# Kernel tuning notes

Hardware: AMD Instinct MI355X
Metric: run time of the kernel (lower is better)

The kernel has to match this reference:

```python
import jax, jax.numpy as jnp
import numpy as np

N, T, C, H = 32, 512, 768, 1536  # batch, seq_len, dim, int(dim*expand)


def setup_inputs() -> dict:
    key = jax.random.key(0)
    ks = jax.random.split(key, 10)
    sc = lambda fan: 1.0 / np.sqrt(fan)
    return {
        "x_seq": jax.random.normal(ks[0], (N, T, C), jnp.float32),
        "sup_seq": jax.random.uniform(ks[1], (N, T, 1), jnp.float32),
        # torch nn.Linear weights are [out, in]; y = x @ W.T + b
        "W_in": jax.random.normal(ks[2], (C, C), jnp.float32) * sc(C),
        "W_out": jax.random.normal(ks[3], (C, C), jnp.float32) * sc(C),
        "W_bg": jax.random.normal(ks[4], (C, C), jnp.float32) * sc(C),
        "b_bg": jax.random.normal(ks[5], (C,), jnp.float32) * 0.01,
        "W_sg": jax.random.normal(ks[6], (C, 1), jnp.float32),
        "b_sg": jax.random.normal(ks[7], (C,), jnp.float32) * 0.01,
        "W_f1": jax.random.normal(ks[8], (H, C), jnp.float32) * sc(C),
        "b_f1": jnp.zeros((H,), jnp.float32),
        "W_f2": jax.random.normal(ks[9], (C, H), jnp.float32) * sc(H),
        "b_f2": jnp.zeros((C,), jnp.float32),
    }


def reference(x_seq, sup_seq, W_in, W_out, W_bg, b_bg, W_sg, b_sg, W_f1, b_f1, W_f2, b_f2):
    # in_proj (no bias)
    x = jnp.einsum('ntc,dc->ntd', x_seq, W_in)                      # [N,T,C]
    # per-step FFN with residual (exact erf GELU, matching torch default)
    h = jax.nn.gelu(jnp.einsum('ntc,hc->nth', x, W_f1) + b_f1, approximate=False)
    xt = x + jnp.einsum('nth,ch->ntc', h, W_f2) + b_f2              # [N,T,C]
    # input-dependent gate (base_gate * sup_to_gate)
    g = jax.nn.sigmoid(jnp.einsum('ntc,dc->ntd', xt, W_bg) + b_bg)
    g = g * jax.nn.sigmoid(jnp.einsum('nto,do->ntd', sup_seq, W_sg) + b_sg)
    # linear recurrence s_t = (1-g_t)*s_{t-1} + g_t*xt_t, s_0 = 0 -> associative scan
    a = 1.0 - g
    b = g * xt

    def combine(c1, c2):
        a1, b1 = c1
        a2, b2 = c2
        return a2 * a1, a2 * b1 + b2

    _, s = jax.lax.associative_scan(combine, (a, b), axis=1)        # [N,T,C]
    return jnp.einsum('ntc,dc->ntd', s, W_out)
```

## Files before the change

kernel.cpp:

```cpp
#include <hip/hip_runtime.h>
#include <hip/hip_bf16.h>
#include <math.h>

typedef __bf16 bf16;
typedef __attribute__((ext_vector_type(8))) __bf16 bf16x8;
typedef __attribute__((ext_vector_type(4))) __bf16 bf16x4;
typedef __attribute__((ext_vector_type(4))) float f32x4;

constexpr int BM = 128, BN = 128, BK = 32;

enum { EPI_PLAIN = 0, EPI_GELU = 1, EPI_RES = 2, EPI_GATE = 3 };

__device__ __forceinline__ void async16(const void* g, void* l) {
  __builtin_amdgcn_global_load_lds(
      (const __attribute__((address_space(1))) void*)g,
      (__attribute__((address_space(3))) void*)l, 16, 0, 0);
}

__device__ __forceinline__ void bar_lgkm() {
  asm volatile("s_waitcnt lgkmcnt(0)\n\ts_barrier" ::: "memory");
}

#define WAIT_VM(n) asm volatile("s_waitcnt vmcnt(" #n ")" ::: "memory")
#define MFMA16(d, va, vb) \
  d = __builtin_amdgcn_mfma_f32_16x16x32_bf16(va, vb, d, 0, 0, 0)

template <typename CT, int EPI>
__global__ __launch_bounds__(256, 2) void gemm_bt_a(
    const bf16* __restrict__ A, const bf16* __restrict__ B, CT* __restrict__ C,
    const float* __restrict__ bias, const bf16* __restrict__ resid,
    const float* __restrict__ sup, const float* __restrict__ wsg,
    const float* __restrict__ bsg, int M, int N, int K) {
  __shared__ bf16 As[2][BM * BK];
  __shared__ bf16 Bs[2][BN * BK];

  const int tid = threadIdx.x;
  const int bm = blockIdx.x, bn = blockIdx.y;
  const int lane = tid & 63;
  const int wv = tid >> 6;
  const int wm = (wv >> 1) * 64, wn = (wv & 1) * 64;
  const int quad = lane >> 4, l16 = lane & 15;

  f32x4 acc[4][4];
#pragma unroll
  for (int i = 0; i < 4; i++)
#pragma unroll
    for (int j = 0; j < 4; j++) acc[i][j] = f32x4{0.f, 0.f, 0.f, 0.f};

  const bf16* Ab = A + (size_t)(bm * BM) * K;
  const bf16* Bb = B + (size_t)(bn * BN) * K;
  const int srow = tid >> 2;
  const int sq8 = ((tid & 3) ^ ((srow >> 1) & 3)) * 8;
  const int slot8 = (quad ^ ((l16 >> 1) & 3)) * 8;

  auto stage = [&](int buf, int kk) {
#pragma unroll
    for (int it = 0; it < 2; ++it) {
      int row = it * 64 + srow;
      async16(Ab + (size_t)row * K + kk + sq8, &As[buf][(it * 256 + wv * 64) * 8]);
    }
#pragma unroll
    for (int it = 0; it < 2; ++it) {
      int row = it * 64 + srow;
      async16(Bb + (size_t)row * K + kk + sq8, &Bs[buf][(it * 256 + wv * 64) * 8]);
    }
  };

  stage(0, 0);

  const int nt = K / BK;
  for (int t = 0; t < nt; ++t) {
    const int cur = t & 1;
    if (t + 1 < nt) {
      stage(cur ^ 1, (t + 1) * BK);
      WAIT_VM(4);
    } else {
      WAIT_VM(0);
    }
    bar_lgkm();

    bf16x8 af[4], bfr[4];
#pragma unroll
    for (int i = 0; i < 4; i++)
      af[i] = *(const bf16x8*)&As[cur][(wm + i * 16 + l16) * BK + slot8];
#pragma unroll
    for (int j = 0; j < 4; j++)
      bfr[j] = *(const bf16x8*)&Bs[cur][(wn + j * 16 + l16) * BK + slot8];
#pragma unroll
    for (int i = 0; i < 4; i++)
#pragma unroll
      for (int j = 0; j < 4; j++)
        acc[i][j] = __builtin_amdgcn_mfma_f32_16x16x32_bf16(af[i], bfr[j], acc[i][j], 0, 0, 0);
    bar_lgkm();
  }

#pragma unroll
  for (int i = 0; i < 4; i++) {
    int row0 = bm * BM + wm + i * 16 + quad * 4;
#pragma unroll
    for (int j = 0; j < 4; j++) {
      int col = bn * BN + wn + j * 16 + l16;
#pragma unroll
      for (int r = 0; r < 4; r++) {
        int row = row0 + r;
        size_t idx = (size_t)row * N + col;
        float v = acc[i][j][r];
        if constexpr (EPI == EPI_PLAIN) {
          C[idx] = (CT)v;
        } else if constexpr (EPI == EPI_GELU) {
          v += bias[col];
          float gl = 0.5f * v * (1.0f + erff(v * 0.70710678118654752f));
          C[idx] = (CT)gl;
        } else if constexpr (EPI == EPI_RES) {
          v += bias[col] + (float)resid[idx];
          C[idx] = (CT)v;
        } else {
          v += bias[col];
          float g1 = 1.0f / (1.0f + expf(-v));
          float z = sup[row] * wsg[col] + bsg[col];
          float g2 = 1.0f / (1.0f + expf(-z));
          C[idx] = (CT)(g1 * g2);
        }
      }
    }
  }
}

constexpr int SC_CH = 32, SC_NCH = 16, SC_CW = 32;

__global__ __launch_bounds__(512) void scan2_kernel(const float* __restrict__ g,
                                                    const bf16* __restrict__ xt,
                                                    bf16* __restrict__ s, int T, int C) {
  __shared__ float lA[SC_NCH][SC_CW];
  __shared__ float lB[SC_NCH][SC_CW];
  __shared__ float lC[SC_NCH][SC_CW];
  const int cl = threadIdx.x & (SC_CW - 1);
  const int ch = threadIdx.x / SC_CW;
  const int c = blockIdx.x * SC_CW + cl;
  const int n = blockIdx.y;
  const size_t base = ((size_t)n * T + ch * SC_CH) * C + c;

  float a_arr[SC_CH], sl[SC_CH];
  float A = 1.f, B = 0.f;
#pragma unroll
  for (int t = 0; t < SC_CH; ++t) {
    size_t idx = base + (size_t)t * C;
    float gv = g[idx], xv = (float)xt[idx];
    float at = 1.0f - gv;
    a_arr[t] = at;
    B = at * B + gv * xv;
    sl[t] = B;
    A *= at;
  }
  lA[ch][cl] = A;
  lB[ch][cl] = B;
  __syncthreads();
  if (ch == 0) {
    float carry = 0.f;
#pragma unroll
    for (int j = 0; j < SC_NCH; ++j) {
      lC[j][cl] = carry;
      carry = lA[j][cl] * carry + lB[j][cl];
    }
  }
  __syncthreads();
  const float carry = lC[ch][cl];
  float P = 1.f;
#pragma unroll
  for (int t = 0; t < SC_CH; ++t) {
    P *= a_arr[t];
    s[base + (size_t)t * C] = (bf16)(sl[t] + P * carry);
  }
}

__global__ __launch_bounds__(256) void cvt5_kernel(
    const float* s0, bf16* d0, int n0, const float* s1, bf16* d1, int n1,
    const float* s2, bf16* d2, int n2, const float* s3, bf16* d3, int n3,
    const float* s4, bf16* d4, int n4) {
  const float* s; bf16* d; int n;
  switch (blockIdx.y) {
    case 0: s = s0; d = d0; n = n0; break;
    case 1: s = s1; d = d1; n = n1; break;
    case 2: s = s2; d = d2; n = n2; break;
    case 3: s = s3; d = d3; n = n3; break;
    default: s = s4; d = d4; n = n4; break;
  }
  int i = blockIdx.x * 256 + threadIdx.x;
  if (i < n) d[i] = (bf16)s[i];
}

__global__ __launch_bounds__(256) void cvtx_kernel(const float* __restrict__ in,
                                                   bf16* __restrict__ out, int n4) {
  int i = blockIdx.x * 256 + threadIdx.x;
  if (i < n4) {
    f32x4 v = *(const f32x4*)(in + (size_t)i * 4);
    bf16x4 b;
    b[0] = (bf16)v[0]; b[1] = (bf16)v[1]; b[2] = (bf16)v[2]; b[3] = (bf16)v[3];
    *(bf16x4*)(out + (size_t)i * 4) = b;
  }
}

extern "C" void kernel_launch(void* const* d_in, const int* in_sizes, int n_in,
                              void* d_out, int out_size, void* d_ws, size_t ws_size,
                              hipStream_t stream) {
  const float* x_seq = (const float*)d_in[0];
  const float* sup = (const float*)d_in[1];
  const float* W_in = (const float*)d_in[2];
  const float* W_out = (const float*)d_in[3];
  const float* W_bg = (const float*)d_in[4];
  const float* b_bg = (const float*)d_in[5];
  const float* W_sg = (const float*)d_in[6];
  const float* b_sg = (const float*)d_in[7];
  const float* W_f1 = (const float*)d_in[8];
  const float* b_f1 = (const float*)d_in[9];
  const float* W_f2 = (const float*)d_in[10];
  const float* b_f2 = (const float*)d_in[11];

  const int Nb = 32, T = 512, C = 768, H = 1536;
  const int M = Nb * T;

  char* ws = (char*)d_ws;
  size_t off = 0;
  auto alloc = [&](size_t bytes) {
    void* p = ws + off;
    off += (bytes + 255) & ~(size_t)255;
    return p;
  };
  bf16* Win_bf = (bf16*)alloc((size_t)C * C * 2);
  bf16* Wf1_bf = (bf16*)alloc((size_t)H * C * 2);
  bf16* Wf2_bf = (bf16*)alloc((size_t)C * H * 2);
  bf16* Wbg_bf = (bf16*)alloc((size_t)C * C * 2);
  bf16* Wout_bf = (bf16*)alloc((size_t)C * C * 2);
  bf16* xs_bf = (bf16*)alloc((size_t)M * C * 2);
  bf16* x_bf = (bf16*)alloc((size_t)M * C * 2);
  bf16* h_bf = (bf16*)alloc((size_t)M * H * 2);
  bf16* xt_bf = (bf16*)alloc((size_t)M * C * 2);
  float* g_f = (float*)alloc((size_t)M * C * 4);
  bf16* s_bf = x_bf;

  cvt5_kernel<<<dim3((H * C + 255) / 256, 5), 256, 0, stream>>>(
      W_in, Win_bf, C * C, W_f1, Wf1_bf, H * C, W_f2, Wf2_bf, C * H,
      W_bg, Wbg_bf, C * C, W_out, Wout_bf, C * C);
  cvtx_kernel<<<(M * C / 4 + 255) / 256, 256, 0, stream>>>(x_seq, xs_bf, M * C / 4);

  dim3 blk(256);
  gemm_bt_a<bf16, EPI_PLAIN><<<dim3(M / BM, C / BN), blk, 0, stream>>>(
      xs_bf, Win_bf, x_bf, nullptr, nullptr, nullptr, nullptr, nullptr, M, C, C);
  gemm_bt_a<bf16, EPI_GELU><<<dim3(M / BM, H / BN), blk, 0, stream>>>(
      x_bf, Wf1_bf, h_bf, b_f1, nullptr, nullptr, nullptr, nullptr, M, H, C);
  gemm_bt_a<bf16, EPI_RES><<<dim3(M / BM, C / BN), blk, 0, stream>>>(
      h_bf, Wf2_bf, xt_bf, b_f2, x_bf, nullptr, nullptr, nullptr, M, C, H);
  gemm_bt_a<float, EPI_GATE><<<dim3(M / BM, C / BN), blk, 0, stream>>>(
      xt_bf, Wbg_bf, g_f, b_bg, nullptr, sup, W_sg, b_sg, M, C, C);
  scan2_kernel<<<dim3(C / SC_CW, Nb), dim3(SC_CW * SC_NCH), 0, stream>>>(
      g_f, xt_bf, s_bf, T, C);
  gemm_bt_a<float, EPI_PLAIN><<<dim3(M / BM, C / BN), blk, 0, stream>>>(
      s_bf, Wout_bf, (float*)d_out, nullptr, nullptr, nullptr, nullptr, nullptr, M, C, C);
}
```

Baseline: 375.9 us.

## Use 8-wave GEMM blocks with XCD-aware 1D tile swizzle

Changes the GEMM kernel from 4 waves with 64x64 warp tiles to 8 waves with 64x32 warp tiles on the same 128x128x32 block tile, so each thread issues one async load per operand per stage instead of two. The grid becomes 1D with a remap that gives each of the 8 XCDs a contiguous range of tiles, which is meant to improve L2 reuse of A/B panels. Pointer increments replace per-stage address recomputation. More waves per block raise latency hiding but halve per-wave MFMA work relative to the LDS reads, which raises LDS traffic per MFMA.

```diff
diff --git a/kernel.cpp b/kernel.cpp
--- a/kernel.cpp
+++ b/kernel.cpp
@@ -22,11 +22,9 @@
 }
 
 #define WAIT_VM(n) asm volatile("s_waitcnt vmcnt(" #n ")" ::: "memory")
-#define MFMA16(d, va, vb) \
-  d = __builtin_amdgcn_mfma_f32_16x16x32_bf16(va, vb, d, 0, 0, 0)
 
 template <typename CT, int EPI>
-__global__ __launch_bounds__(256, 2) void gemm_bt_a(
+__global__ __launch_bounds__(512, 4) void gemm_bt_a(
     const bf16* __restrict__ A, const bf16* __restrict__ B, CT* __restrict__ C,
     const float* __restrict__ bias, const bf16* __restrict__ resid,
     const float* __restrict__ sup, const float* __restrict__ wsg,
@@ -35,61 +33,64 @@
   __shared__ bf16 Bs[2][BN * BK];
 
   const int tid = threadIdx.x;
-  const int bm = blockIdx.x, bn = blockIdx.y;
+  const int nwg = gridDim.x;
+  const int cpx = nwg >> 3;
+  const int wg = blockIdx.x;
+  const int sw = (wg & 7) * cpx + (wg >> 3);
+  const int ntn = N >> 7;
+  const int bm = sw / ntn, bn = sw - bm * ntn;
+
   const int lane = tid & 63;
   const int wv = tid >> 6;
-  const int wm = (wv >> 1) * 64, wn = (wv & 1) * 64;
+  const int wm = (wv >> 2) * 64, wn = (wv & 3) * 32;
   const int quad = lane >> 4, l16 = lane & 15;
 
-  f32x4 acc[4][4];
+  f32x4 acc[4][2];
 #pragma unroll
   for (int i = 0; i < 4; i++)
 #pragma unroll
-    for (int j = 0; j < 4; j++) acc[i][j] = f32x4{0.f, 0.f, 0.f, 0.f};
-
-  const bf16* Ab = A + (size_t)(bm * BM) * K;
-  const bf16* Bb = B + (size_t)(bn * BN) * K;
+    for (int j = 0; j < 2; j++) acc[i][j] = f32x4{0.f, 0.f, 0.f, 0.f};
+
   const int srow = tid >> 2;
   const int sq8 = ((tid & 3) ^ ((srow >> 1) & 3)) * 8;
   const int slot8 = (quad ^ ((l16 >> 1) & 3)) * 8;
 
-  auto stage = [&](int buf, int kk) {
-#pragma unroll
-    for (int it = 0; it < 2; ++it) {
-      int row = it * 64 + srow;
-      async16(Ab + (size_t)row * K + kk + sq8, &As[buf][(it * 256 + wv * 64) * 8]);
-    }
-#pragma unroll
-    for (int it = 0; it < 2; ++it) {
-      int row = it * 64 + srow;
-      async16(Bb + (size_t)row * K + kk + sq8, &Bs[buf][(it * 256 + wv * 64) * 8]);
-    }
+  const bf16* pa = A + (size_t)(bm * BM + srow) * K + sq8;
+  const bf16* pb = B + (size_t)(bn * BN + srow) * K + sq8;
+  bf16* dA = &As[0][0] + wv * 512;
+  bf16* dB = &Bs[0][0] + wv * 512;
+
+  auto stg = [&](int buf) {
+    async16(pa, dA + buf * 4096);
+    async16(pb, dB + buf * 4096);
+    pa += BK;
+    pb += BK;
   };
 
-  stage(0, 0);
+  stg(0);
 
   const int nt = K / BK;
   for (int t = 0; t < nt; ++t) {
     const int cur = t & 1;
     if (t + 1 < nt) {
-      stage(cur ^ 1, (t + 1) * BK);
-      WAIT_VM(4);
+      stg(cur ^ 1);
+      WAIT_VM(2);
     } else {
       WAIT_VM(0);
     }
     bar_lgkm();
 
-    bf16x8 af[4], bfr[4];
+    bf16x8 af[4], bfr[2];
 #pragma unroll
     for (int i = 0; i < 4; i++)
       af[i] = *(const bf16x8*)&As[cur][(wm + i * 16 + l16) * BK + slot8];
 #pragma unroll
-    for (int j = 0; j < 4; j++)
+    for (int j = 0; j < 2; j++)
       bfr[j] = *(const bf16x8*)&Bs[cur][(wn + j * 16 + l16) * BK + slot8];
 #pragma unroll
     for (int i = 0; i < 4; i++)
 #pragma unroll
-      for (int j = 0; j < 4; j++)
+      for (int j = 0; j < 2; j++)
         acc[i][j] = __builtin_amdgcn_mfma_f32_16x16x32_bf16(af[i], bfr[j], acc[i][j], 0, 0, 0);
     bar_lgkm();
   }
@@ -98,7 +99,7 @@
   for (int i = 0; i < 4; i++) {
     int row0 = bm * BM + wm + i * 16 + quad * 4;
 #pragma unroll
-    for (int j = 0; j < 4; j++) {
+    for (int j = 0; j < 2; j++) {
       int col = bn * BN + wn + j * 16 + l16;
 #pragma unroll
       for (int r = 0; r < 4; r++) {
@@ -243,17 +244,17 @@
       W_bg, Wbg_bf, C * C, W_out, Wout_bf, C * C);
   cvtx_kernel<<<(M * C / 4 + 255) / 256, 256, 0, stream>>>(x_seq, xs_bf, M * C / 4);
 
-  dim3 blk(256);
-  gemm_bt_a<bf16, EPI_PLAIN><<<dim3(M / BM, C / BN), blk, 0, stream>>>(
+  dim3 blk(512);
+  gemm_bt_a<bf16, EPI_PLAIN><<<dim3((M / BM) * (C / BN)), blk, 0, stream>>>(
       xs_bf, Win_bf, x_bf, nullptr, nullptr, nullptr, nullptr, nullptr, M, C, C);
-  gemm_bt_a<bf16, EPI_GELU><<<dim3(M / BM, H / BN), blk, 0, stream>>>(
+  gemm_bt_a<bf16, EPI_GELU><<<dim3((M / BM) * (H / BN)), blk, 0, stream>>>(
       x_bf, Wf1_bf, h_bf, b_f1, nullptr, nullptr, nullptr, nullptr, M, H, C);
-  gemm_bt_a<bf16, EPI_RES><<<dim3(M / BM, C / BN), blk, 0, stream>>>(
+  gemm_bt_a<bf16, EPI_RES><<<dim3((M / BM) * (C / BN)), blk, 0, stream>>>(
       h_bf, Wf2_bf, xt_bf, b_f2, x_bf, nullptr, nullptr, nullptr, M, C, H);
-  gemm_bt_a<float, EPI_GATE><<<dim3(M / BM, C / BN), blk, 0, stream>>>(
+  gemm_bt_a<float, EPI_GATE><<<dim3((M / BM) * (C / BN)), blk, 0, stream>>>(
       xt_bf, Wbg_bf, g_f, b_bg, nullptr, sup, W_sg, b_sg, M, C, C);
   scan2_kernel<<<dim3(C / SC_CW, Nb), dim3(SC_CW * SC_NCH), 0, stream>>>(
       g_f, xt_bf, s_bf, T, C);
-  gemm_bt_a<float, EPI_PLAIN><<<dim3(M / BM, C / BN), blk, 0, stream>>>(
+  gemm_bt_a<float, EPI_PLAIN><<<dim3((M / BM) * (C / BN)), blk, 0, stream>>>(
       s_bf, Wout_bf, (float*)d_out, nullptr, nullptr, nullptr, nullptr, nullptr, M, C, C);
 }
```

Result: no change. 378.9 us (+0.8%).
